# Kernel optimization log

Measured on AMD Instinct MI355X. Metric: run time of the kernel, lower is better.

The kernel has to match this reference:

```python
import jax, jax.numpy as jnp
import numpy as np

H, DH = 16, 64  # heads, dim_head (inner_dim = 1024)


def _sdpa(q, k, v):
    # q: (B, Q, D), k/v: (B, K, D); scale = 1/sqrt(D) as in F.scaled_dot_product_attention
    scale = 1.0 / jnp.sqrt(jnp.asarray(q.shape[-1], q.dtype))
    s = jnp.einsum('bqd,bkd->bqk', q, k) * scale
    return jnp.einsum('bqk,bkd->bqd', jax.nn.softmax(s, axis=-1), v)


def setup_inputs() -> dict:
    key = jax.random.key(0)
    ks = jax.random.split(key, 3)
    b, f, n, dim = 8, 16, 196, 1024
    N = 1 + f * n  # CLS + frames*patches = 3137
    x = jax.random.normal(ks[0], (b, N, dim), jnp.float32)
    w_qkv = jax.random.normal(ks[1], (3 * H * DH, dim), jnp.float32) * 0.02
    w_out = jax.random.normal(ks[2], (dim, H * DH), jnp.float32) * 0.02
    b_out = jnp.zeros((dim,), jnp.float32)
    return {"x": x, "w_qkv": w_qkv, "w_out": w_out, "b_out": b_out, "f": f}


def reference(x, w_qkv, w_out, b_out, f):
    b, N, dim = x.shape
    n = (N - 1) // f  # patches per frame

    qkv = x @ w_qkv.T  # (b, N, 3*H*DH)
    q, k, v = jnp.split(qkv, 3, axis=-1)

    def to_bh(t):  # 'b n (h d) -> (b h) n d'
        return t.reshape(b, N, H, DH).transpose(0, 2, 1, 3).reshape(b * H, N, DH)

    q, k, v = map(to_bh, (q, k, v))

    cls_q, q_ = q[:, :1], q[:, 1:]
    cls_k, k_ = k[:, :1], k[:, 1:]
    cls_v, v_ = v[:, :1], v[:, 1:]

    # CLS token attends over all tokens
    cls_out = _sdpa(cls_q, k, v)  # (b*H, 1, DH)

    # spatial attention: '(b h) (f n) d -> (b h f) n d'
    def to_space(t):
        return t.reshape(b * H, f, n, DH).reshape(b * H * f, n, DH)

    q_, k_, v_ = map(to_space, (q_, k_, v_))

    # repeat_interleave CLS k/v over the f groups, then prepend
    ck = jnp.repeat(cls_k, f, axis=0)  # (b*H*f, 1, DH)
    cv = jnp.repeat(cls_v, f, axis=0)
    k_ = jnp.concatenate((ck, k_), axis=1)  # (b*H*f, n+1, DH)
    v_ = jnp.concatenate((cv, v_), axis=1)

    out = _sdpa(q_, k_, v_)  # (b*H*f, n, DH)
    out = out.reshape(b * H, f * n, DH)  # '(b f) n d -> b (f n) d'
    out = jnp.concatenate((cls_out, out), axis=1)  # (b*H, N, DH)
    # '(b h) n d -> b n (h d)'
    out = out.reshape(b, H, N, DH).transpose(0, 2, 1, 3).reshape(b, N, H * DH)
    return out @ w_out.T + b_out
```

## Files before the change

### kernel.cpp

```cpp
#include <hip/hip_runtime.h>
#include <cstdint>
#include <cstddef>

#define DEVINL __device__ __forceinline__

typedef __attribute__((ext_vector_type(8))) short short8;
typedef __attribute__((ext_vector_type(4))) float f32x4;
typedef unsigned short u16;
typedef unsigned int u32;

DEVINL u16 f2b(float f) {
    u32 u = __float_as_uint(f);
    u32 r = (u + 0x7fffu + ((u >> 16) & 1u)) >> 16;
    return (u16)r;
}
DEVINL float b2f(u16 h) { return __uint_as_float(((u32)h) << 16); }

DEVINL void gl_lds16(const void* g, void* l) {
    __builtin_amdgcn_global_load_lds(
        (const __attribute__((address_space(1))) void*)g,
        (__attribute__((address_space(3))) void*)l, 16, 0, 0);
}

#define MROWS   25096
#define NTOK    3137
#define QE      25698304
#define LOG2E   1.4426950408889634f

__global__ __launch_bounds__(256) void cvt_kernel(const float* __restrict__ in,
                                                  u16* __restrict__ out, int n4) {
    int i = blockIdx.x * blockDim.x + threadIdx.x;
    int stride = gridDim.x * blockDim.x;
    for (int j = i; j < n4; j += stride) {
        float4 v = ((const float4*)in)[j];
        ushort4 o;
        o.x = f2b(v.x); o.y = f2b(v.y); o.z = f2b(v.z); o.w = f2b(v.w);
        ((ushort4*)out)[j] = o;
    }
}


#define LDS_BUF 32768
#define NTILES  16

template <int MODE>
__global__ __launch_bounds__(512, 2) void gemm256(const u16* __restrict__ A,
                                                  const u16* __restrict__ B,
                                                  u16* __restrict__ q_out,
                                                  u16* __restrict__ k_out,
                                                  u16* __restrict__ v_out,
                                                  const float* __restrict__ bias,
                                                  float* __restrict__ f_out, int M) {
    __shared__ u16 lds[2 * LDS_BUF];
    const int tid = threadIdx.x, lane = tid & 63, w = tid >> 6;
    const int Mm1 = M - 1;

    const u32 nwg = gridDim.x * gridDim.y;
    const u32 orig = blockIdx.y * gridDim.x + blockIdx.x;
    const u32 q8 = nwg >> 3, r8 = nwg & 7, xcd = orig & 7, rest = orig >> 3;
    const u32 wg = (xcd < r8 ? xcd * (q8 + 1) : r8 * (q8 + 1) + (xcd - r8) * q8) + rest;
    const int m0 = (int)(wg / gridDim.x) * 256;
    const int n0 = (int)(wg % gridDim.x) * 256;

    const int wm = w >> 2, wn = w & 3;

    const int stRow = lane >> 2;
    const int stCol = (((lane & 3) ^ ((lane >> 3) & 3)) << 3);

    const int slotOff = (((lane >> 4) ^ ((lane >> 1) & 3)) << 3);
    const int rdA = (wm * 128 + (lane & 15)) * 32 + slotOff;
    const int rdB = (wn * 64 + (lane & 15)) * 32 + slotOff + 16384;

#define STAGE_A(NB, KK, KT) do {                                              \
    _Pragma("unroll") for (int j_ = 0; j_ < 2; ++j_) {                        \
        const int c_ = (w << 1) | j_;                                         \
        int r_ = m0 + c_ * 16 + stRow; if (r_ > Mm1) r_ = Mm1;                \
        gl_lds16(A + (size_t)r_ * 1024 + (KT) + (KK) * 32 + stCol,            \
                 lds + (NB) + (KK) * 8192 + c_ * 512);                        \
    } } while (0)

#define STAGE_B(NB, KK, KT) do {                                              \
    _Pragma("unroll") for (int j_ = 0; j_ < 2; ++j_) {                        \
        const int c_ = (w << 1) | j_;                                         \
        const int r_ = n0 + c_ * 16 + stRow;                                  \
        gl_lds16(B + (size_t)r_ * 1024 + (KT) + (KK) * 32 + stCol,            \
                 lds + (NB) + 16384 + (KK) * 8192 + c_ * 512);                \
    } } while (0)

#define LDA4(CB, KK, MB) do {                                                 \
    _Pragma("unroll") for (int i_ = 0; i_ < 4; ++i_)                          \
        aF[i_] = *(const short8*)&lds[(CB) + (KK) * 8192 + rdA +              \
                                      ((MB) + i_) * 16 * 32];                 \
    } while (0)

#define LDB4(CB, KK) do {                                                     \
    _Pragma("unroll") for (int i_ = 0; i_ < 4; ++i_)                          \
        bF[i_] = *(const short8*)&lds[(CB) + (KK) * 8192 + rdB +              \
                                      i_ * 16 * 32];                          \
    } while (0)

#define MFMA16(MB) do {                                                       \
    _Pragma("unroll") for (int i_ = 0; i_ < 4; ++i_)                          \
        _Pragma("unroll") for (int n_ = 0; n_ < 4; ++n_)                      \
            acc[(MB) + i_][n_] = __builtin_amdgcn_mfma_f32_16x16x32_bf16(     \
                aF[i_], bF[n_], acc[(MB) + i_][n_], 0, 0, 0);                 \
    } while (0)

#define LGKM0_FENCE() do {                                                    \
    asm volatile("s_waitcnt lgkmcnt(0)" ::: "memory");                        \
    __builtin_amdgcn_sched_barrier(0); } while (0)

    f32x4 acc[8][4];
    const f32x4 zf = {0.f, 0.f, 0.f, 0.f};
#pragma unroll
    for (int i = 0; i < 8; ++i)
#pragma unroll
        for (int j = 0; j < 4; ++j) acc[i][j] = zf;

    STAGE_A(0, 0, 0);
    STAGE_B(0, 0, 0);
    STAGE_A(0, 1, 0);
    STAGE_B(0, 1, 0);
    asm volatile("s_waitcnt vmcnt(4)" ::: "memory");
    __builtin_amdgcn_sched_barrier(0);
    __builtin_amdgcn_s_barrier();

    for (int T = 0; T < NTILES; ++T) {
        const int cb = (T & 1) * LDS_BUF;
        const int nb = ((T + 1) & 1) * LDS_BUF;
        const bool pf = (T < NTILES - 1);
        const int kt1 = (T + 1) * 64;

        short8 aF[4], bF[4];

        LDA4(cb, 0, 0);
        LDB4(cb, 0);
        if (pf) STAGE_A(nb, 0, kt1);
        __builtin_amdgcn_s_barrier();
        LGKM0_FENCE();
        __builtin_amdgcn_s_setprio(1);
        MFMA16(0);
        __builtin_amdgcn_s_setprio(0);
        __builtin_amdgcn_s_barrier();

        LDA4(cb, 0, 4);
        if (pf) STAGE_B(nb, 0, kt1);
        __builtin_amdgcn_s_barrier();
        LGKM0_FENCE();
        __builtin_amdgcn_s_setprio(1);
        MFMA16(4);
        __builtin_amdgcn_s_setprio(0);
        if (pf) { asm volatile("s_waitcnt vmcnt(4)" ::: "memory"); }
        else    { asm volatile("s_waitcnt vmcnt(0)" ::: "memory"); }
        __builtin_amdgcn_sched_barrier(0);
        __builtin_amdgcn_s_barrier();

        LDA4(cb, 1, 0);
        LDB4(cb, 1);
        if (pf) STAGE_A(nb, 1, kt1);
        __builtin_amdgcn_s_barrier();
        LGKM0_FENCE();
        __builtin_amdgcn_s_setprio(1);
        MFMA16(0);
        __builtin_amdgcn_s_setprio(0);
        __builtin_amdgcn_s_barrier();

        LDA4(cb, 1, 4);
        if (pf) STAGE_B(nb, 1, kt1);
        __builtin_amdgcn_s_barrier();
        LGKM0_FENCE();
        __builtin_amdgcn_s_setprio(1);
        MFMA16(4);
        __builtin_amdgcn_s_setprio(0);
        if (pf) {
            asm volatile("s_waitcnt vmcnt(4)" ::: "memory");
            __builtin_amdgcn_sched_barrier(0);
        }
        __builtin_amdgcn_s_barrier();
    }

#pragma unroll
    for (int m = 0; m < 8; ++m) {
#pragma unroll
        for (int n = 0; n < 4; ++n) {
#pragma unroll
            for (int r = 0; r < 4; ++r) {
                const int gm = m0 + wm * 128 + m * 16 + ((lane >> 4) << 2) + r;
                if (gm < M) {
                    const int gc = n0 + wn * 64 + n * 16 + (lane & 15);
                    if (MODE == 0) {
                        const int t = gc >> 10;
                        const int h = (gc >> 6) & 15;
                        const int d = gc & 63;
                        const u32 bb = (u32)gm / 3137u;
                        const u32 nn = (u32)gm - bb * 3137u;
                        u16* dst = (t == 0) ? q_out : (t == 1) ? k_out : v_out;
                        dst[(((size_t)(bb * 16 + h)) * NTOK + nn) * 64 + d] =
                            f2b(acc[m][n][r]);
                    } else {
                        f_out[(size_t)gm * 1024 + gc] = acc[m][n][r] + bias[gc];
                    }
                }
            }
        }
    }
#undef STAGE_A
#undef STAGE_B
#undef LDA4
#undef LDB4
#undef MFMA16
#undef LGKM0_FENCE
}

#define CSZ 393
__global__ __launch_bounds__(256) void attn_cls_part(const u16* __restrict__ qb,
                                                     const u16* __restrict__ kb,
                                                     const u16* __restrict__ vb,
                                                     float* __restrict__ part) {
    const int bid = blockIdx.x;
    const int bh = bid >> 3, c = bid & 7;
    const size_t base = (size_t)bh * NTOK * 64;
    const int tid = threadIdx.x, lane = tid & 63, wid = tid >> 6;
    const int j0 = c * CSZ;
    const int cnt = min(NTOK - j0, CSZ);

    __shared__ float qs[64];
    __shared__ float sc[CSZ];
    __shared__ float redbuf[8];
    __shared__ float ored[4][64];

    if (tid < 64) qs[tid] = b2f(qb[base + tid]);
    __syncthreads();

    for (int j = tid; j < cnt; j += 256) {
        const u16* kr = kb + base + (size_t)(j0 + j) * 64;
        float acc = 0.f;
#pragma unroll
        for (int c2 = 0; c2 < 8; ++c2) {
            short8 v8 = *(const short8*)(kr + c2 * 8);
#pragma unroll
            for (int t = 0; t < 8; ++t) acc += qs[c2 * 8 + t] * b2f((u16)v8[t]);
        }
        sc[j] = acc * 0.125f;
    }
    __syncthreads();

    float mx = -1e30f;
    for (int j = tid; j < cnt; j += 256) mx = fmaxf(mx, sc[j]);
#pragma unroll
    for (int m = 32; m >= 1; m >>= 1) mx = fmaxf(mx, __shfl_xor(mx, m));
    if (lane == 0) redbuf[wid] = mx;
    __syncthreads();
    mx = fmaxf(fmaxf(redbuf[0], redbuf[1]), fmaxf(redbuf[2], redbuf[3]));

    float sum = 0.f;
    for (int j = tid; j < cnt; j += 256) {
        float p = exp2f((sc[j] - mx) * LOG2E);
        sc[j] = p;
        sum += p;
    }
#pragma unroll
    for (int m = 32; m >= 1; m >>= 1) sum += __shfl_xor(sum, m);
    if (lane == 0) redbuf[4 + wid] = sum;
    __syncthreads();
    const float tot = redbuf[4] + redbuf[5] + redbuf[6] + redbuf[7];

    const int d = tid & 63, g = tid >> 6;
    float o = 0.f;
    for (int j = g; j < cnt; j += 4)
        o += sc[j] * b2f(vb[base + (size_t)(j0 + j) * 64 + d]);
    ored[g][d] = o;
    __syncthreads();

    float* pb = part + (size_t)bid * 66;
    if (tid < 64) pb[2 + tid] = ored[0][tid] + ored[1][tid] + ored[2][tid] + ored[3][tid];
    else if (tid == 64) pb[0] = mx;
    else if (tid == 65) pb[1] = tot;
}

__global__ __launch_bounds__(64) void attn_cls_fin(const float* __restrict__ part,
                                                   u16* __restrict__ attnb) {
    const int bh = blockIdx.x, d = threadIdx.x;
    const int bb = bh >> 4, h = bh & 15;
    float m = -1e30f;
#pragma unroll
    for (int c = 0; c < 8; ++c) m = fmaxf(m, part[(size_t)(bh * 8 + c) * 66]);
    float t = 0.f, o = 0.f;
#pragma unroll
    for (int c = 0; c < 8; ++c) {
        const float* pb = part + (size_t)(bh * 8 + c) * 66;
        const float w = exp2f((pb[0] - m) * LOG2E);
        t += w * pb[1];
        o += w * pb[2 + d];
    }
    attnb[(size_t)bb * NTOK * 1024 + h * 64 + d] = f2b(o / t);
}

__global__ __launch_bounds__(256) void attn_spatial(const u16* __restrict__ qb,
                                                    const u16* __restrict__ kb,
                                                    const u16* __restrict__ vb,
                                                    u16* __restrict__ attnb) {
    const int blk = blockIdx.x;
    const int bh = blk >> 4, fi = blk & 15;
    const int bb = bh >> 4, h = bh & 15;
    const int tid = threadIdx.x, lane = tid & 63, wid = tid >> 6;
    const int hi = lane >> 4, lo = lane & 15;
    const size_t kvbase = (size_t)bh * NTOK * 64;

    __shared__ u16 Kl[197 * 72];
    __shared__ u16 Vt[64 * 208];
    __shared__ u16 Pl[4 * 16 * 208];

    u16* Ptmp = Pl;
    for (int idx = tid; idx < 197 * 8; idx += 256) {
        const int j = idx >> 3, c = idx & 7;
        const int n = (j == 0) ? 0 : (1 + fi * 196 + (j - 1));
        *(short8*)(Kl + j * 72 + c * 8) =
            *(const short8*)(kb + kvbase + (size_t)n * 64 + c * 8);
        *(short8*)(Ptmp + ((j * 64 + c * 8) ^ ((j & 7) << 3))) =
            *(const short8*)(vb + kvbase + (size_t)n * 64 + c * 8);
    }
    __syncthreads();
#pragma unroll
    for (int c = 0; c < 8; ++c) {
        if (tid < 197) {
            short8 v8 = *(const short8*)(Ptmp + ((tid * 64 + c * 8) ^ ((tid & 7) << 3)));
#pragma unroll
            for (int t = 0; t < 8; ++t) Vt[(c * 8 + t) * 208 + tid] = (u16)v8[t];
        }
    }
    for (int idx = tid; idx < 64 * 11; idx += 256)
        Vt[(idx / 11) * 208 + 197 + (idx % 11)] = 0;
    __syncthreads();

    u16* pl = Pl + wid * 16 * 208;
    const short8 z8 = {0, 0, 0, 0, 0, 0, 0, 0};
    const f32x4 zf = {0.f, 0.f, 0.f, 0.f};

    for (int mf = wid; mf < 13; mf += 4) {
        int qr = mf * 16 + lo; if (qr > 195) qr = 195;
        const u16* qp = qb + kvbase + (size_t)(1 + fi * 196 + qr) * 64 + hi * 8;
        const short8 a0 = *(const short8*)(qp);
        const short8 a1 = *(const short8*)(qp + 32);

        f32x4 s[13];
#pragma unroll
        for (int nf = 0; nf < 13; ++nf) s[nf] = zf;
#pragma unroll
        for (int nf = 0; nf < 13; ++nf) {
            int kr = nf * 16 + lo; if (kr > 196) kr = 196;
            const u16* kp = Kl + kr * 72 + hi * 8;
            const short8 b0 = *(const short8*)(kp);
            const short8 b1 = *(const short8*)(kp + 32);
            s[nf] = __builtin_amdgcn_mfma_f32_16x16x32_bf16(a0, b0, s[nf], 0, 0, 0);
            s[nf] = __builtin_amdgcn_mfma_f32_16x16x32_bf16(a1, b1, s[nf], 0, 0, 0);
        }

        float rls[4];
#pragma unroll
        for (int reg = 0; reg < 4; ++reg) {
            float mx = -1e30f;
#pragma unroll
            for (int nf = 0; nf < 13; ++nf) {
                const int col = nf * 16 + lo;
                float v = s[nf][reg] * 0.125f;
                if (col >= 197) v = -1e30f;
                s[nf][reg] = v;
                mx = fmaxf(mx, v);
            }
            mx = fmaxf(mx, __shfl_xor(mx, 1));
            mx = fmaxf(mx, __shfl_xor(mx, 2));
            mx = fmaxf(mx, __shfl_xor(mx, 4));
            mx = fmaxf(mx, __shfl_xor(mx, 8));
            float sum = 0.f;
#pragma unroll
            for (int nf = 0; nf < 13; ++nf) {
                const float p = exp2f((s[nf][reg] - mx) * LOG2E);
                s[nf][reg] = p;
                sum += p;
            }
            sum += __shfl_xor(sum, 1);
            sum += __shfl_xor(sum, 2);
            sum += __shfl_xor(sum, 4);
            sum += __shfl_xor(sum, 8);
            rls[reg] = 1.0f / sum;
        }

#pragma unroll
        for (int nf = 0; nf < 13; ++nf)
#pragma unroll
            for (int reg = 0; reg < 4; ++reg)
                pl[(hi * 4 + reg) * 208 + nf * 16 + lo] = f2b(s[nf][reg]);

        f32x4 o[4];
#pragma unroll
        for (int i = 0; i < 4; ++i) o[i] = zf;
#pragma unroll
        for (int kk = 0; kk < 6; ++kk) {
            const short8 pa = *(const short8*)(pl + lo * 208 + kk * 32 + hi * 8);
#pragma unroll
            for (int nf2 = 0; nf2 < 4; ++nf2) {
                const short8 bvv =
                    *(const short8*)(Vt + (nf2 * 16 + lo) * 208 + kk * 32 + hi * 8);
                o[nf2] = __builtin_amdgcn_mfma_f32_16x16x32_bf16(pa, bvv, o[nf2], 0, 0, 0);
            }
        }
        {
            const u16* pap = pl + lo * 208 + 192 + (hi < 2 ? hi * 8 : 0);
            short8 pa = *(const short8*)pap;
            if (hi >= 2) pa = z8;
#pragma unroll
            for (int nf2 = 0; nf2 < 4; ++nf2) {
                const u16* bvp = Vt + (nf2 * 16 + lo) * 208 + 192 + (hi < 2 ? hi * 8 : 0);
                short8 bvv = *(const short8*)bvp;
                if (hi >= 2) bvv = z8;
                o[nf2] = __builtin_amdgcn_mfma_f32_16x16x32_bf16(pa, bvv, o[nf2], 0, 0, 0);
            }
        }

#pragma unroll
        for (int nf2 = 0; nf2 < 4; ++nf2)
#pragma unroll
            for (int reg = 0; reg < 4; ++reg) {
                const int r = mf * 16 + hi * 4 + reg;
                if (r < 196) {
                    const int d = nf2 * 16 + lo;
                    const size_t nn = 1 + fi * 196 + r;
                    attnb[((size_t)bb * NTOK + nn) * 1024 + h * 64 + d] =
                        f2b(o[nf2][reg] * rls[reg]);
                }
            }
    }
}

extern "C" void kernel_launch(void* const* d_in, const int* in_sizes, int n_in,
                              void* d_out, int out_size, void* d_ws, size_t ws_size,
                              hipStream_t stream) {
    const float* x = (const float*)d_in[0];
    const float* w_qkv = (const float*)d_in[1];
    const float* w_out = (const float*)d_in[2];
    const float* b_out = (const float*)d_in[3];

    const size_t need = ((size_t)QE * 2 + 3145728 + 1048576) * 2;
    if (ws_size < need) {
        hipMemsetAsync(d_out, 0, (size_t)out_size * 4, stream);
        return;
    }

    u16* vb = (u16*)d_ws;
    u16* xab = vb + QE;
    u16* wqb = xab + QE;
    u16* wob = wqb + 3145728;
    u16* qb = (u16*)d_out;
    u16* kb = qb + QE;
    float* outf = (float*)d_out;
    float* clsp = (float*)wqb;

    cvt_kernel<<<2048, 256, 0, stream>>>(x, xab, QE / 4);
    cvt_kernel<<<2048, 256, 0, stream>>>(w_qkv, wqb, 3145728 / 4);
    cvt_kernel<<<1024, 256, 0, stream>>>(w_out, wob, 1048576 / 4);

    gemm256<0><<<dim3(12, 99), 512, 0, stream>>>(xab, wqb, qb, kb, vb, nullptr,
                                                 nullptr, MROWS);
    attn_cls_part<<<1024, 256, 0, stream>>>(qb, kb, vb, clsp);
    attn_cls_fin<<<128, 64, 0, stream>>>(clsp, xab);
    attn_spatial<<<2048, 256, 0, stream>>>(qb, kb, vb, xab);
    gemm256<1><<<dim3(4, 99), 512, 0, stream>>>(xab, wob, nullptr, nullptr, nullptr,
                                                b_out, outf, MROWS);
}
```

Measured before the change: 465.2 us.

## Switch GEMM inner loop to 32x32x16 MFMA and halve barrier phases

Replaces the 16x16x32 bf16 MFMA tiling with 32x32x16 MFMAs (4x2 fragments per wave), changing the LDS fragment read addressing and swizzle, the accumulator layout and the epilogue row/column mapping. Each K-half now loads all A/B fragments at once and issues the A and B prefetch together, cutting the number of barrier-separated phases per tile from four to two. The goal is fewer LDS reads per FLOP and less barrier overhead. The cost is more live fragment registers and less interleaving of prefetch with compute.

```diff
diff --git a/kernel.cpp b/kernel.cpp
--- a/kernel.cpp
+++ b/kernel.cpp
@@ -6,6 +6,7 @@
 
 typedef __attribute__((ext_vector_type(8))) short short8;
 typedef __attribute__((ext_vector_type(4))) float f32x4;
+typedef __attribute__((ext_vector_type(16))) float f32x16;
 typedef unsigned short u16;
 typedef unsigned int u32;
 
@@ -67,9 +68,11 @@
     const int stRow = lane >> 2;
     const int stCol = (((lane & 3) ^ ((lane >> 3) & 3)) << 3);
 
-    const int slotOff = (((lane >> 4) ^ ((lane >> 1) & 3)) << 3);
-    const int rdA = (wm * 128 + (lane & 15)) * 32 + slotOff;
-    const int rdB = (wn * 64 + (lane & 15)) * 32 + slotOff + 16384;
+    const int fsw = (lane >> 1) & 3;
+    const int phys0 = (((lane >> 5)) ^ fsw) << 3;
+    const int phys1 = ((2 + (lane >> 5)) ^ fsw) << 3;
+    const int rowA = (wm * 128 + (lane & 31)) * 32;
+    const int rowB = (wn * 64 + (lane & 31)) * 32 + 16384;
 
 #define STAGE_A(NB, KK, KT) do {                                              \
     _Pragma("unroll") for (int j_ = 0; j_ < 2; ++j_) {                        \
@@ -87,35 +90,40 @@
                  lds + (NB) + 16384 + (KK) * 8192 + c_ * 512);                \
     } } while (0)
 
-#define LDA4(CB, KK, MB) do {                                                 \
-    _Pragma("unroll") for (int i_ = 0; i_ < 4; ++i_)                          \
-        aF[i_] = *(const short8*)&lds[(CB) + (KK) * 8192 + rdA +              \
-                                      ((MB) + i_) * 16 * 32];                 \
-    } while (0)
-
-#define LDB4(CB, KK) do {                                                     \
-    _Pragma("unroll") for (int i_ = 0; i_ < 4; ++i_)                          \
-        bF[i_] = *(const short8*)&lds[(CB) + (KK) * 8192 + rdB +              \
-                                      i_ * 16 * 32];                          \
-    } while (0)
-
-#define MFMA16(MB) do {                                                       \
-    _Pragma("unroll") for (int i_ = 0; i_ < 4; ++i_)                          \
-        _Pragma("unroll") for (int n_ = 0; n_ < 4; ++n_)                      \
-            acc[(MB) + i_][n_] = __builtin_amdgcn_mfma_f32_16x16x32_bf16(     \
-                aF[i_], bF[n_], acc[(MB) + i_][n_], 0, 0, 0);                 \
+#define LDFRAGS(CB, PH) do {                                                  \
+    _Pragma("unroll") for (int mf_ = 0; mf_ < 4; ++mf_) {                     \
+        aF[mf_]     = *(const short8*)&lds[(CB) + (PH) * 8192 + rowA +        \
+                                           mf_ * 1024 + phys0];               \
+        aF[4 + mf_] = *(const short8*)&lds[(CB) + (PH) * 8192 + rowA +        \
+                                           mf_ * 1024 + phys1];               \
+    }                                                                         \
+    _Pragma("unroll") for (int nf_ = 0; nf_ < 2; ++nf_) {                     \
+        bF[nf_]     = *(const short8*)&lds[(CB) + (PH) * 8192 + rowB +        \
+                                           nf_ * 1024 + phys0];               \
+        bF[2 + nf_] = *(const short8*)&lds[(CB) + (PH) * 8192 + rowB +        \
+                                           nf_ * 1024 + phys1];               \
+    } } while (0)
+
+#define MFMA16() do {                                                         \
+    _Pragma("unroll") for (int ks_ = 0; ks_ < 2; ++ks_)                       \
+        _Pragma("unroll") for (int mf_ = 0; mf_ < 4; ++mf_)                   \
+            _Pragma("unroll") for (int nf_ = 0; nf_ < 2; ++nf_)               \
+                acc[mf_][nf_] = __builtin_amdgcn_mfma_f32_32x32x16_bf16(      \
+                    aF[ks_ * 4 + mf_], bF[ks_ * 2 + nf_], acc[mf_][nf_],      \
+                    0, 0, 0);                                                 \
     } while (0)
 
 #define LGKM0_FENCE() do {                                                    \
     asm volatile("s_waitcnt lgkmcnt(0)" ::: "memory");                        \
     __builtin_amdgcn_sched_barrier(0); } while (0)
 
-    f32x4 acc[8][4];
-    const f32x4 zf = {0.f, 0.f, 0.f, 0.f};
-#pragma unroll
-    for (int i = 0; i < 8; ++i)
-#pragma unroll
-        for (int j = 0; j < 4; ++j) acc[i][j] = zf;
+    f32x16 acc[4][2];
+#pragma unroll
+    for (int i = 0; i < 4; ++i)
+#pragma unroll
+        for (int j = 0; j < 2; ++j)
+#pragma unroll
+            for (int e = 0; e < 16; ++e) acc[i][j][e] = 0.f;
 
     STAGE_A(0, 0, 0);
     STAGE_B(0, 0, 0);
@@ -131,46 +139,26 @@
         const bool pf = (T < NTILES - 1);
         const int kt1 = (T + 1) * 64;
 
-        short8 aF[4], bF[4];
-
-        LDA4(cb, 0, 0);
-        LDB4(cb, 0);
-        if (pf) STAGE_A(nb, 0, kt1);
+        short8 aF[8], bF[4];
+
+        LDFRAGS(cb, 0);
+        if (pf) { STAGE_A(nb, 0, kt1); STAGE_B(nb, 0, kt1); }
         __builtin_amdgcn_s_barrier();
         LGKM0_FENCE();
         __builtin_amdgcn_s_setprio(1);
-        MFMA16(0);
-        __builtin_amdgcn_s_setprio(0);
-        __builtin_amdgcn_s_barrier();
-
-        LDA4(cb, 0, 4);
-        if (pf) STAGE_B(nb, 0, kt1);
-        __builtin_amdgcn_s_barrier();
-        LGKM0_FENCE();
-        __builtin_amdgcn_s_setprio(1);
-        MFMA16(4);
+        MFMA16();
         __builtin_amdgcn_s_setprio(0);
         if (pf) { asm volatile("s_waitcnt vmcnt(4)" ::: "memory"); }
         else    { asm volatile("s_waitcnt vmcnt(0)" ::: "memory"); }
         __builtin_amdgcn_sched_barrier(0);
         __builtin_amdgcn_s_barrier();
 
-        LDA4(cb, 1, 0);
-        LDB4(cb, 1);
-        if (pf) STAGE_A(nb, 1, kt1);
+        LDFRAGS(cb, 1);
+        if (pf) { STAGE_A(nb, 1, kt1); STAGE_B(nb, 1, kt1); }
         __builtin_amdgcn_s_barrier();
         LGKM0_FENCE();
         __builtin_amdgcn_s_setprio(1);
-        MFMA16(0);
-        __builtin_amdgcn_s_setprio(0);
-        __builtin_amdgcn_s_barrier();
-
-        LDA4(cb, 1, 4);
-        if (pf) STAGE_B(nb, 1, kt1);
-        __builtin_amdgcn_s_barrier();
-        LGKM0_FENCE();
-        __builtin_amdgcn_s_setprio(1);
-        MFMA16(4);
+        MFMA16();
         __builtin_amdgcn_s_setprio(0);
         if (pf) {
             asm volatile("s_waitcnt vmcnt(4)" ::: "memory");
@@ -180,25 +168,29 @@
     }
 
 #pragma unroll
-    for (int m = 0; m < 8; ++m) {
-#pragma unroll
-        for (int n = 0; n < 4; ++n) {
-#pragma unroll
-            for (int r = 0; r < 4; ++r) {
-                const int gm = m0 + wm * 128 + m * 16 + ((lane >> 4) << 2) + r;
-                if (gm < M) {
-                    const int gc = n0 + wn * 64 + n * 16 + (lane & 15);
-                    if (MODE == 0) {
-                        const int t = gc >> 10;
-                        const int h = (gc >> 6) & 15;
-                        const int d = gc & 63;
-                        const u32 bb = (u32)gm / 3137u;
-                        const u32 nn = (u32)gm - bb * 3137u;
-                        u16* dst = (t == 0) ? q_out : (t == 1) ? k_out : v_out;
-                        dst[(((size_t)(bb * 16 + h)) * NTOK + nn) * 64 + d] =
-                            f2b(acc[m][n][r]);
-                    } else {
-                        f_out[(size_t)gm * 1024 + gc] = acc[m][n][r] + bias[gc];
+    for (int mf = 0; mf < 4; ++mf) {
+#pragma unroll
+        for (int nf = 0; nf < 2; ++nf) {
+#pragma unroll
+            for (int q = 0; q < 4; ++q) {
+#pragma unroll
+                for (int e = 0; e < 4; ++e) {
+                    const int row = e + q * 8 + ((lane >> 5) << 2);
+                    const int gm = m0 + wm * 128 + mf * 32 + row;
+                    if (gm < M) {
+                        const int gc = n0 + wn * 64 + nf * 32 + (lane & 31);
+                        const float val = acc[mf][nf][q * 4 + e];
+                        if (MODE == 0) {
+                            const int t = gc >> 10;
+                            const int h = (gc >> 6) & 15;
+                            const int d = gc & 63;
+                            const u32 bb = (u32)gm / 3137u;
+                            const u32 nn = (u32)gm - bb * 3137u;
+                            u16* dst = (t == 0) ? q_out : (t == 1) ? k_out : v_out;
+                            dst[(((size_t)(bb * 16 + h)) * NTOK + nn) * 64 + d] = f2b(val);
+                        } else {
+                            f_out[(size_t)gm * 1024 + gc] = val + bias[gc];
+                        }
                     }
                 }
             }
@@ -206,8 +198,7 @@
     }
 #undef STAGE_A
 #undef STAGE_B
-#undef LDA4
-#undef LDB4
+#undef LDFRAGS
 #undef MFMA16
 #undef LGKM0_FENCE
 }
```

Measured after the change: 489.2 us. +5.2%, slower.

## Front-load GEMM next-tile prefetch and remove masking from spatial attention softmax

Applied to the files above, without the earlier changes.

In the pipelined GEMM loop, the A and B loads for both halves of the next K-tile are now issued in the first two sub-phases instead of being spread across all four. The wait is relaxed to vmcnt(8) to match, so global loads get more time to overlap with MFMA work. In the spatial attention kernel, K is zero-padded to 208 rows with a 68-element stride, which removes the clamping and column masking. The 1/sqrt(d) scale is folded into the exp2 argument, and the known contribution of the 11 padded zero-score keys is subtracted from the softmax denominator. Risks: the 136-byte K row stride may break 16-byte alignment of the vector LDS reads, and the subtraction can cost some precision.

```diff
diff --git a/kernel.cpp b/kernel.cpp
--- a/kernel.cpp
+++ b/kernel.cpp
@@ -26,6 +26,7 @@
 #define NTOK    3137
 #define QE      25698304
 #define LOG2E   1.4426950408889634f
+#define SCL2    0.1803368801111204f
 
 __global__ __launch_bounds__(256) void cvt_kernel(const float* __restrict__ in,
                                                   u16* __restrict__ out, int n4) {
@@ -135,7 +136,7 @@
 
         LDA4(cb, 0, 0);
         LDB4(cb, 0);
-        if (pf) STAGE_A(nb, 0, kt1);
+        if (pf) { STAGE_A(nb, 0, kt1); STAGE_B(nb, 0, kt1); }
         __builtin_amdgcn_s_barrier();
         LGKM0_FENCE();
         __builtin_amdgcn_s_setprio(1);
@@ -144,20 +145,19 @@
         __builtin_amdgcn_s_barrier();
 
         LDA4(cb, 0, 4);
-        if (pf) STAGE_B(nb, 0, kt1);
+        if (pf) { STAGE_A(nb, 1, kt1); STAGE_B(nb, 1, kt1); }
         __builtin_amdgcn_s_barrier();
         LGKM0_FENCE();
         __builtin_amdgcn_s_setprio(1);
         MFMA16(4);
         __builtin_amdgcn_s_setprio(0);
-        if (pf) { asm volatile("s_waitcnt vmcnt(4)" ::: "memory"); }
+        if (pf) { asm volatile("s_waitcnt vmcnt(8)" ::: "memory"); }
         else    { asm volatile("s_waitcnt vmcnt(0)" ::: "memory"); }
         __builtin_amdgcn_sched_barrier(0);
         __builtin_amdgcn_s_barrier();
 
         LDA4(cb, 1, 0);
         LDB4(cb, 1);
-        if (pf) STAGE_A(nb, 1, kt1);
         __builtin_amdgcn_s_barrier();
         LGKM0_FENCE();
         __builtin_amdgcn_s_setprio(1);
@@ -166,7 +166,6 @@
         __builtin_amdgcn_s_barrier();
 
         LDA4(cb, 1, 4);
-        if (pf) STAGE_B(nb, 1, kt1);
         __builtin_amdgcn_s_barrier();
         LGKM0_FENCE();
         __builtin_amdgcn_s_setprio(1);
@@ -307,18 +306,22 @@
     const int hi = lane >> 4, lo = lane & 15;
     const size_t kvbase = (size_t)bh * NTOK * 64;
 
-    __shared__ u16 Kl[197 * 72];
+    __shared__ u16 Kl[208 * 68];
     __shared__ u16 Vt[64 * 208];
     __shared__ u16 Pl[4 * 16 * 208];
 
     u16* Ptmp = Pl;
-    for (int idx = tid; idx < 197 * 8; idx += 256) {
+    const short8 z8 = {0, 0, 0, 0, 0, 0, 0, 0};
+    for (int idx = tid; idx < 208 * 8; idx += 256) {
         const int j = idx >> 3, c = idx & 7;
-        const int n = (j == 0) ? 0 : (1 + fi * 196 + (j - 1));
-        *(short8*)(Kl + j * 72 + c * 8) =
-            *(const short8*)(kb + kvbase + (size_t)n * 64 + c * 8);
-        *(short8*)(Ptmp + ((j * 64 + c * 8) ^ ((j & 7) << 3))) =
-            *(const short8*)(vb + kvbase + (size_t)n * 64 + c * 8);
+        short8 kval = z8;
+        if (j < 197) {
+            const int n = (j == 0) ? 0 : (1 + fi * 196 + (j - 1));
+            kval = *(const short8*)(kb + kvbase + (size_t)n * 64 + c * 8);
+            *(short8*)(Ptmp + ((j * 64 + c * 8) ^ ((j & 7) << 3))) =
+                *(const short8*)(vb + kvbase + (size_t)n * 64 + c * 8);
+        }
+        *(short8*)(Kl + j * 68 + c * 8) = kval;
     }
     __syncthreads();
 #pragma unroll
@@ -334,7 +337,6 @@
     __syncthreads();
 
     u16* pl = Pl + wid * 16 * 208;
-    const short8 z8 = {0, 0, 0, 0, 0, 0, 0, 0};
     const f32x4 zf = {0.f, 0.f, 0.f, 0.f};
 
     for (int mf = wid; mf < 13; mf += 4) {
@@ -348,8 +350,7 @@
         for (int nf = 0; nf < 13; ++nf) s[nf] = zf;
 #pragma unroll
         for (int nf = 0; nf < 13; ++nf) {
-            int kr = nf * 16 + lo; if (kr > 196) kr = 196;
-            const u16* kp = Kl + kr * 72 + hi * 8;
+            const u16* kp = Kl + (nf * 16 + lo) * 68 + hi * 8;
             const short8 b0 = *(const short8*)(kp);
             const short8 b1 = *(const short8*)(kp + 32);
             s[nf] = __builtin_amdgcn_mfma_f32_16x16x32_bf16(a0, b0, s[nf], 0, 0, 0);
@@ -359,23 +360,18 @@
         float rls[4];
 #pragma unroll
         for (int reg = 0; reg < 4; ++reg) {
-            float mx = -1e30f;
-#pragma unroll
-            for (int nf = 0; nf < 13; ++nf) {
-                const int col = nf * 16 + lo;
-                float v = s[nf][reg] * 0.125f;
-                if (col >= 197) v = -1e30f;
-                s[nf][reg] = v;
-                mx = fmaxf(mx, v);
-            }
+            float mx = s[0][reg];
+#pragma unroll
+            for (int nf = 1; nf < 13; ++nf) mx = fmaxf(mx, s[nf][reg]);
             mx = fmaxf(mx, __shfl_xor(mx, 1));
             mx = fmaxf(mx, __shfl_xor(mx, 2));
             mx = fmaxf(mx, __shfl_xor(mx, 4));
             mx = fmaxf(mx, __shfl_xor(mx, 8));
+            const float mC = mx * SCL2;
             float sum = 0.f;
 #pragma unroll
             for (int nf = 0; nf < 13; ++nf) {
-                const float p = exp2f((s[nf][reg] - mx) * LOG2E);
+                const float p = exp2f(fmaf(s[nf][reg], SCL2, -mC));
                 s[nf][reg] = p;
                 sum += p;
             }
@@ -383,7 +379,7 @@
             sum += __shfl_xor(sum, 2);
             sum += __shfl_xor(sum, 4);
             sum += __shfl_xor(sum, 8);
-            rls[reg] = 1.0f / sum;
+            rls[reg] = 1.0f / (sum - 11.0f * exp2f(-mC));
         }
 
 #pragma unroll
```

After: 517.3 us. +11.2%, slower.
